# Kernel tuning notes

Measured on AMD Instinct MI355X. Metric: run time of the kernel, lower is better.

The kernel has to match this reference:

```python
import jax, jax.numpy as jnp
import numpy as np

K = 2
NOISE_STD = 1.0

def setup_inputs() -> dict:
    key = jax.random.key(0)
    k1, k2, k3 = jax.random.split(key, 3)
    N, D, E = 131072, 1024, 64
    x = jax.random.normal(k1, (N, D), dtype=jnp.float32)
    W = jax.random.normal(k2, (E, D), dtype=jnp.float32) * (1.0 / np.sqrt(D))
    b = jnp.zeros((E,), dtype=jnp.float32)
    noise = jax.random.normal(k3, (N, E), dtype=jnp.float32)
    return {"x": x, "W": W, "b": b, "noise": noise}

def reference(x, W, b, noise) -> jnp.ndarray:
    # clean logits: [N, E]
    clean_logits = jnp.einsum('nd,ed->ne', x, W) + b
    noisy_logits = clean_logits + noise * NOISE_STD
    topk_vals, topk_idx = jax.lax.top_k(noisy_logits, K)  # [N, K]
    topk_softmax = jax.nn.softmax(topk_vals, axis=-1)     # [N, K]
    rows = jnp.arange(x.shape[0])[:, None]                 # [N, 1]
    gate_weights = jnp.zeros_like(clean_logits).at[rows, topk_idx].set(topk_softmax)
    return gate_weights
```

## Files before the change

kernel.cpp:

```cpp
#include <hip/hip_runtime.h>
#include <math.h>


#define NEXP   64
#define BLOCK  256
#define TILE_M 64
#define DFIX   1024
#define KCF    128
#define NCH    8
#define XCHB   32768
#define TAU    1e-3f
#define CAP    4096
#define WS_W_OFF 32768

typedef __attribute__((ext_vector_type(8)))  short bf16x8;
typedef __attribute__((ext_vector_type(16))) float f32x16;

__device__ __forceinline__ bool beats(float v, int e, float vo, int eo) {
    return (v > vo) || (v == vo && e < eo);
}

__device__ __forceinline__ void split2(float f0, float f1, unsigned int& hi, unsigned int& lo) {
    unsigned int u0 = __float_as_uint(f0), u1 = __float_as_uint(f1);
    unsigned int h0 = u0 & 0xFFFF0000u,  h1 = u1 & 0xFFFF0000u;
    float l0 = f0 - __uint_as_float(h0);
    float l1 = f1 - __uint_as_float(h1);
    hi = (u0 >> 16) | h1;
    lo = (__float_as_uint(l0) >> 16) | (__float_as_uint(l1) & 0xFFFF0000u);
}

__device__ __forceinline__ void gl_lds16(const void* g, void* l) {
    __builtin_amdgcn_global_load_lds((const __attribute__((address_space(1))) void*)g,
                                     (__attribute__((address_space(3))) void*)l,
                                     16, 0, 0);
}

__global__ void convW_kernel(const float* __restrict__ W, char* __restrict__ wsW) {
    const int e = blockIdx.x;
    const int t = threadIdx.x;
    const float* wp = W + e * DFIX + t * 8;
    float4 a  = *(const float4*)wp;
    float4 bq = *(const float4*)(wp + 4);
    unsigned int h[4], l[4];
    split2(a.x,  a.y,  h[0], l[0]);
    split2(a.z,  a.w,  h[1], l[1]);
    split2(bq.x, bq.y, h[2], l[2]);
    split2(bq.z, bq.w, h[3], l[3]);
    const int kk   = t >> 1;
    const int lh   = t & 1;
    const int lane = lh * 32 + (e & 31);
    const int g    = e >> 5;
    char* base = wsW + (size_t)(kk * 4 + g * 2) * 1024 + lane * 16;
    *(uint4*)(base)        = make_uint4(h[0], h[1], h[2], h[3]);
    *(uint4*)(base + 1024) = make_uint4(l[0], l[1], l[2], l[3]);
}

__global__ __launch_bounds__(BLOCK, 2)
void gate_mfma(const float* __restrict__ x, const float* __restrict__ bvec,
               const float* __restrict__ noise, const char* __restrict__ wsW,
               float* __restrict__ out, unsigned int* __restrict__ flags) {
    __shared__ __align__(16) char lds[2 * XCHB];

    const int tid  = threadIdx.x;
    const int wv   = tid >> 6;
    const int lane = tid & 63;
    const int e0   = lane & 31;
    const int lh   = lane >> 5;
    const int rg   = wv & 1;
    const int cg   = wv >> 1;
    const int blkRow0 = blockIdx.x * TILE_M;
    const int rowL  = rg * 32 + e0;
    const int phase = blockIdx.x & (NCH - 1);

    f32x16 acc = (f32x16)0.0f;

    auto STAGE = [&](int gc, int buf) {
        char* xb = lds + buf * XCHB;
        #pragma unroll
        for (int j = 0; j < 8; j++) {
            const int s   = j * 256 + wv * 64 + lane;
            const int row = s >> 5;
            const int seg = (s & 31) ^ (row & 31);
            const char* gp = (const char*)(x + (size_t)(blkRow0 + row) * DFIX)
                             + (size_t)gc * 512 + seg * 16;
            gl_lds16(gp, xb + (size_t)(j * 256 + wv * 64) * 16);
        }
    };

    int4 wreg[16];
    auto WPRE = [&](int gc) {
        const char* base = wsW + (size_t)(gc * 32 + cg * 2) * 1024 + lane * 16;
        #pragma unroll
        for (int ks = 0; ks < 8; ks++) {
            wreg[ks * 2 + 0] = *(const int4*)(base + (ks * 4 + 0) * 1024);
            wreg[ks * 2 + 1] = *(const int4*)(base + (ks * 4 + 1) * 1024);
        }
    };

    auto COMPUTE = [&](int buf) {
        const char* xb = lds + buf * XCHB;
        #pragma unroll
        for (int ks = 0; ks < 8; ks++) {
            const int g0 = ks * 4 + lh * 2;
            const int4 xq0 = *(const int4*)(xb + rowL * 512 + ((g0    ) ^ (rowL & 31)) * 16);
            const int4 xq1 = *(const int4*)(xb + rowL * 512 + ((g0 + 1) ^ (rowL & 31)) * 16);
            const float4 xa = *(const float4*)&xq0;
            const float4 xc = *(const float4*)&xq1;
            union { bf16x8 v; unsigned int u[4]; } ah, al;
            split2(xa.x, xa.y, ah.u[0], al.u[0]);
            split2(xa.z, xa.w, ah.u[1], al.u[1]);
            split2(xc.x, xc.y, ah.u[2], al.u[2]);
            split2(xc.z, xc.w, ah.u[3], al.u[3]);
            union { bf16x8 v; int4 q; } bh, bl;
            bh.q = wreg[ks * 2 + 0];
            bl.q = wreg[ks * 2 + 1];
            acc = __builtin_amdgcn_mfma_f32_32x32x16_bf16(ah.v, bh.v, acc, 0, 0, 0);
            acc = __builtin_amdgcn_mfma_f32_32x32x16_bf16(ah.v, bl.v, acc, 0, 0, 0);
            acc = __builtin_amdgcn_mfma_f32_32x32x16_bf16(al.v, bh.v, acc, 0, 0, 0);
        }
    };

    STAGE(phase, 0);
    #pragma unroll 1
    for (int c = 0; c < NCH - 1; c++) {
        WPRE((c + phase) & (NCH - 1));
        STAGE((c + 1 + phase) & (NCH - 1), (c + 1) & 1);
        asm volatile("s_waitcnt vmcnt(8)" ::: "memory");
        __builtin_amdgcn_s_barrier();
        __builtin_amdgcn_sched_barrier(0);
        COMPUTE(c & 1);
        __builtin_amdgcn_s_barrier();
    }
    WPRE((NCH - 1 + phase) & (NCH - 1));
    asm volatile("s_waitcnt vmcnt(0)" ::: "memory");
    __builtin_amdgcn_s_barrier();
    __builtin_amdgcn_sched_barrier(0);
    COMPUTE((NCH - 1) & 1);

    const float bb = bvec[cg * 32 + e0];
    #pragma unroll
    for (int q = 0; q < 4; q++) {
        #pragma unroll
        for (int j = 0; j < 4; j++) {
            const int reg = q * 4 + j;
            const int rl  = rg * 32 + j + 8 * q + 4 * lh;
            const int r   = blkRow0 + rl;
            const int col = cg * 32 + e0;
            const float v = (acc[reg] + bb) + noise[(size_t)r * NEXP + col];
            const int slot = (col >> 2) ^ (rl & 15);
            *(float*)(lds + rl * 256 + slot * 16 + (col & 3) * 4) = v;
        }
    }
    __syncthreads();

    {
        const int trow = tid >> 2;
        const int qd   = tid & 3;
        float v1 = -1e30f, v2 = -1e30f, v3 = -1e30f;
        int   e1 = 99, e2 = 99;
        #pragma unroll
        for (int i = 0; i < 4; i++) {
            const int slot = (qd * 4 + i) ^ (trow & 15);
            const float4 f = *(const float4*)(lds + trow * 256 + slot * 16);
            #pragma unroll
            for (int m = 0; m < 4; m++) {
                const float v = (m == 0) ? f.x : (m == 1) ? f.y : (m == 2) ? f.z : f.w;
                const int   e = qd * 16 + i * 4 + m;
                if (beats(v, e, v1, e1))      { v3 = v2; v2 = v1; e2 = e1; v1 = v; e1 = e; }
                else if (beats(v, e, v2, e2)) { v3 = v2; v2 = v;  e2 = e; }
                else                          { v3 = fmaxf(v3, v); }
            }
        }
        #pragma unroll
        for (int d = 1; d < 4; d <<= 1) {
            float ov1 = __shfl_xor(v1, d); int oe1 = __shfl_xor(e1, d);
            float ov2 = __shfl_xor(v2, d); int oe2 = __shfl_xor(e2, d);
            float ov3 = __shfl_xor(v3, d);
            bool  aw  = beats(v1, e1, ov1, oe1);
            float a1v = aw ? v1 : ov1; int a1e = aw ? e1 : oe1;
            float b1v = aw ? ov1 : v1; int b1e = aw ? oe1 : e1;
            float a2v = aw ? v2 : ov2; int a2e = aw ? e2 : oe2;
            float b2v = aw ? ov2 : v2;
            float a3v = aw ? v3 : ov3;
            bool  s2  = beats(a2v, a2e, b1v, b1e);
            v1 = a1v; e1 = a1e;
            v2 = s2 ? a2v : b1v; e2 = s2 ? a2e : b1e;
            v3 = s2 ? fmaxf(a3v, b1v) : fmaxf(a2v, b2v);
        }
        const float t   = __expf(v2 - v1);
        const float inv = 1.0f / (1.0f + t);
        const float w1  = inv, w2 = t * inv;
        const int   r   = blkRow0 + trow;

        if (qd == 0 && (v2 - v3) < TAU) {
            unsigned int idx = atomicAdd(flags, 1u);
            if (idx < CAP) flags[1 + idx] = (unsigned int)r;
        }
        float* op = out + (size_t)r * NEXP + qd * 16;
        #pragma unroll
        for (int i = 0; i < 4; i++) {
            float o[4];
            #pragma unroll
            for (int m = 0; m < 4; m++) {
                const int e = qd * 16 + i * 4 + m;
                o[m] = (e == e1) ? w1 : (e == e2) ? w2 : 0.0f;
            }
            *(float4*)(op + i * 4) = make_float4(o[0], o[1], o[2], o[3]);
        }
    }
}

__global__ void gate_repair(const float* __restrict__ x, const float* __restrict__ W,
                            const float* __restrict__ b, const float* __restrict__ noise,
                            float* __restrict__ out, const unsigned int* __restrict__ flags,
                            int D) {
    unsigned int cnt = flags[0];
    if (cnt > CAP) cnt = CAP;
    if (blockIdx.x >= cnt) return;
    const int r = (int)flags[1 + blockIdx.x];
    const int e = threadIdx.x;

    const float* xr = x + (size_t)r * D;
    const float* wr = W + (size_t)e * D;
    double s = 0.0;
    for (int d0 = 0; d0 < D; d0 += 4) {
        float4 xv = *(const float4*)(xr + d0);
        float4 wv = *(const float4*)(wr + d0);
        s += (double)xv.x * (double)wv.x;
        s += (double)xv.y * (double)wv.y;
        s += (double)xv.z * (double)wv.z;
        s += (double)xv.w * (double)wv.w;
    }
    const float clean = (float)s + b[e];
    const float v     = clean + noise[(size_t)r * NEXP + e];

    float v1 = v, v2 = -1e30f; int e1 = e, e2 = 99;
    for (int d = 1; d < 64; d <<= 1) {
        float ov1 = __shfl_xor(v1, d); int oe1 = __shfl_xor(e1, d);
        float ov2 = __shfl_xor(v2, d); int oe2 = __shfl_xor(e2, d);
        bool  aw  = beats(v1, e1, ov1, oe1);
        float a1v = aw ? v1 : ov1; int a1e = aw ? e1 : oe1;
        float b1v = aw ? ov1 : v1; int b1e = aw ? oe1 : e1;
        float a2v = aw ? v2 : ov2; int a2e = aw ? e2 : oe2;
        bool  s2  = beats(a2v, a2e, b1v, b1e);
        v1 = a1v; e1 = a1e;
        v2 = s2 ? a2v : b1v; e2 = s2 ? a2e : b1e;
    }
    const float t   = __expf(v2 - v1);
    const float inv = 1.0f / (1.0f + t);
    out[(size_t)r * NEXP + e] = (e == e1) ? inv : (e == e2) ? t * inv : 0.0f;
}

extern "C" void kernel_launch(void* const* d_in, const int* in_sizes, int n_in,
                              void* d_out, int out_size, void* d_ws, size_t ws_size,
                              hipStream_t stream) {
    const float* x     = (const float*)d_in[0];
    const float* W     = (const float*)d_in[1];
    const float* b     = (const float*)d_in[2];
    const float* noise = (const float*)d_in[3];
    float* out = (float*)d_out;

    const int E = in_sizes[2];
    const int D = in_sizes[1] / E;
    const int N = in_sizes[0] / D;

    unsigned int* flags = (unsigned int*)d_ws;
    char* wsW = (char*)d_ws + WS_W_OFF;

    convW_kernel<<<dim3(E), dim3(128), 0, stream>>>(W, wsW);
    hipMemsetAsync(d_ws, 0, sizeof(unsigned int), stream);
    gate_mfma<<<dim3(N / TILE_M), dim3(BLOCK), 0, stream>>>(x, b, noise, wsW, out, flags);
    gate_repair<<<dim3(CAP), dim3(64), 0, stream>>>(x, W, b, noise, out, flags, D);
}
```

Baseline: 204.8 us.

## Double K-chunk size to 256 and load W fragments inline during compute

Each staged x chunk now covers 256 columns instead of 128, giving four pipeline stages instead of eight and a 128 KB double-buffered LDS footprint, with occupancy lowered to one block per CU. The register-prefetched W fragments are dropped and W is read from global memory inside the compute loop right before each MFMA. The intent is fewer barriers and larger, better-amortized loads, but it gives up occupancy and puts W global-load latency directly on the MFMA path.

```diff
diff --git a/kernel.cpp b/kernel.cpp
--- a/kernel.cpp
+++ b/kernel.cpp
@@ -6,9 +6,9 @@
 #define BLOCK  256
 #define TILE_M 64
 #define DFIX   1024
-#define KCF    128
-#define NCH    8
-#define XCHB   32768
+#define KCF    256
+#define NCH    4
+#define XCHB   65536
 #define TAU    1e-3f
 #define CAP    4096
 #define WS_W_OFF 32768
@@ -55,7 +55,7 @@
     *(uint4*)(base + 1024) = make_uint4(l[0], l[1], l[2], l[3]);
 }
 
-__global__ __launch_bounds__(BLOCK, 2)
+__global__ __launch_bounds__(BLOCK, 1)
 void gate_mfma(const float* __restrict__ x, const float* __restrict__ bvec,
                const float* __restrict__ noise, const char* __restrict__ wsW,
                float* __restrict__ out, unsigned int* __restrict__ flags) {
@@ -77,33 +77,27 @@
     auto STAGE = [&](int gc, int buf) {
         char* xb = lds + buf * XCHB;
         #pragma unroll
-        for (int j = 0; j < 8; j++) {
-            const int s   = j * 256 + wv * 64 + lane;
-            const int row = s >> 5;
-            const int seg = (s & 31) ^ (row & 31);
+        for (int i = 0; i < 16; i++) {
+            const int row = wv * 16 + i;
+            const int seg = lane ^ row;
             const char* gp = (const char*)(x + (size_t)(blkRow0 + row) * DFIX)
-                             + (size_t)gc * 512 + seg * 16;
-            gl_lds16(gp, xb + (size_t)(j * 256 + wv * 64) * 16);
+                             + (size_t)gc * 1024 + seg * 16;
+            gl_lds16(gp, xb + (size_t)(wv * 1024 + i * 64) * 16);
         }
     };
 
-    int4 wreg[16];
-    auto WPRE = [&](int gc) {
-        const char* base = wsW + (size_t)(gc * 32 + cg * 2) * 1024 + lane * 16;
-        #pragma unroll
-        for (int ks = 0; ks < 8; ks++) {
-            wreg[ks * 2 + 0] = *(const int4*)(base + (ks * 4 + 0) * 1024);
-            wreg[ks * 2 + 1] = *(const int4*)(base + (ks * 4 + 1) * 1024);
-        }
-    };
-
-    auto COMPUTE = [&](int buf) {
+    auto COMPUTE = [&](int gc, int buf) {
         const char* xb = lds + buf * XCHB;
         #pragma unroll
-        for (int ks = 0; ks < 8; ks++) {
+        for (int ks = 0; ks < 16; ks++) {
+            const int kkg = gc * 16 + ks;
+            const char* wbase = wsW + (size_t)(kkg * 4 + cg * 2) * 1024 + lane * 16;
+            union { bf16x8 v; int4 q; } bh, bl;
+            bh.q = *(const int4*)(wbase);
+            bl.q = *(const int4*)(wbase + 1024);
             const int g0 = ks * 4 + lh * 2;
-            const int4 xq0 = *(const int4*)(xb + rowL * 512 + ((g0    ) ^ (rowL & 31)) * 16);
-            const int4 xq1 = *(const int4*)(xb + rowL * 512 + ((g0 + 1) ^ (rowL & 31)) * 16);
+            const int4 xq0 = *(const int4*)(xb + rowL * 1024 + ((g0    ) ^ rowL) * 16);
+            const int4 xq1 = *(const int4*)(xb + rowL * 1024 + ((g0 + 1) ^ rowL) * 16);
             const float4 xa = *(const float4*)&xq0;
             const float4 xc = *(const float4*)&xq1;
             union { bf16x8 v; unsigned int u[4]; } ah, al;
@@ -111,9 +105,6 @@
             split2(xa.z, xa.w, ah.u[1], al.u[1]);
             split2(xc.x, xc.y, ah.u[2], al.u[2]);
             split2(xc.z, xc.w, ah.u[3], al.u[3]);
-            union { bf16x8 v; int4 q; } bh, bl;
-            bh.q = wreg[ks * 2 + 0];
-            bl.q = wreg[ks * 2 + 1];
             acc = __builtin_amdgcn_mfma_f32_32x32x16_bf16(ah.v, bh.v, acc, 0, 0, 0);
             acc = __builtin_amdgcn_mfma_f32_32x32x16_bf16(ah.v, bl.v, acc, 0, 0, 0);
             acc = __builtin_amdgcn_mfma_f32_32x32x16_bf16(al.v, bh.v, acc, 0, 0, 0);
@@ -123,19 +114,17 @@
     STAGE(phase, 0);
     #pragma unroll 1
     for (int c = 0; c < NCH - 1; c++) {
-        WPRE((c + phase) & (NCH - 1));
         STAGE((c + 1 + phase) & (NCH - 1), (c + 1) & 1);
-        asm volatile("s_waitcnt vmcnt(8)" ::: "memory");
+        asm volatile("s_waitcnt vmcnt(16)" ::: "memory");
         __builtin_amdgcn_s_barrier();
         __builtin_amdgcn_sched_barrier(0);
-        COMPUTE(c & 1);
+        COMPUTE((c + phase) & (NCH - 1), c & 1);
         __builtin_amdgcn_s_barrier();
     }
-    WPRE((NCH - 1 + phase) & (NCH - 1));
     asm volatile("s_waitcnt vmcnt(0)" ::: "memory");
     __builtin_amdgcn_s_barrier();
     __builtin_amdgcn_sched_barrier(0);
-    COMPUTE((NCH - 1) & 1);
+    COMPUTE((NCH - 1 + phase) & (NCH - 1), (NCH - 1) & 1);
 
     const float bb = bvec[cg * 32 + e0];
     #pragma unroll
```

Result: slower. 314.8 us (+53.7%).

## Halve row tile and split K across waves with LDS reduction

Applied to the files above, without the earlier changes.

Shrinks the row tile from 64 to 32 rows. The four waves now split the K dimension in two halves and the expert columns in two halves, and the two K-halves are summed through LDS before the bias, noise and top-k epilogue. This doubles the grid size and widens each staged chunk to 256 columns across 4 chunks. The aim is more blocks for occupancy and load balance, at the cost of an extra LDS reduction and more barriers, with each W fragment reused over fewer rows. Scheduling barriers are also added around the prefetch and staging code.

```diff
diff --git a/kernel.cpp b/kernel.cpp
--- a/kernel.cpp
+++ b/kernel.cpp
@@ -4,11 +4,11 @@
 
 #define NEXP   64
 #define BLOCK  256
-#define TILE_M 64
+#define TILE_M 32
 #define DFIX   1024
-#define KCF    128
-#define NCH    8
+#define NCH    4
 #define XCHB   32768
+#define TK_OFF 8192
 #define TAU    1e-3f
 #define CAP    4096
 #define WS_W_OFF 32768
@@ -66,10 +66,10 @@
     const int lane = tid & 63;
     const int e0   = lane & 31;
     const int lh   = lane >> 5;
-    const int rg   = wv & 1;
-    const int cg   = wv >> 1;
+    const int cg   = wv & 1;
+    const int kh   = wv >> 1;
     const int blkRow0 = blockIdx.x * TILE_M;
-    const int rowL  = rg * 32 + e0;
+    const int rowL  = e0;
     const int phase = blockIdx.x & (NCH - 1);
 
     f32x16 acc = (f32x16)0.0f;
@@ -77,23 +77,23 @@
     auto STAGE = [&](int gc, int buf) {
         char* xb = lds + buf * XCHB;
         #pragma unroll
-        for (int j = 0; j < 8; j++) {
-            const int s   = j * 256 + wv * 64 + lane;
-            const int row = s >> 5;
-            const int seg = (s & 31) ^ (row & 31);
+        for (int i = 0; i < 8; i++) {
+            const int row = wv * 8 + i;
+            const int seg = lane ^ row;
             const char* gp = (const char*)(x + (size_t)(blkRow0 + row) * DFIX)
-                             + (size_t)gc * 512 + seg * 16;
-            gl_lds16(gp, xb + (size_t)(j * 256 + wv * 64) * 16);
+                             + (size_t)gc * 1024 + seg * 16;
+            gl_lds16(gp, xb + (size_t)(row * 64) * 16);
         }
     };
 
     int4 wreg[16];
     auto WPRE = [&](int gc) {
-        const char* base = wsW + (size_t)(gc * 32 + cg * 2) * 1024 + lane * 16;
+        const int kk0 = gc * 16 + kh * 8;
+        const char* base = wsW + (size_t)(kk0 * 4 + cg * 2) * 1024 + lane * 16;
         #pragma unroll
         for (int ks = 0; ks < 8; ks++) {
-            wreg[ks * 2 + 0] = *(const int4*)(base + (ks * 4 + 0) * 1024);
-            wreg[ks * 2 + 1] = *(const int4*)(base + (ks * 4 + 1) * 1024);
+            wreg[ks * 2 + 0] = *(const int4*)(base + (size_t)(ks * 4) * 1024);
+            wreg[ks * 2 + 1] = *(const int4*)(base + (size_t)(ks * 4) * 1024 + 1024);
         }
     };
 
@@ -101,9 +101,10 @@
         const char* xb = lds + buf * XCHB;
         #pragma unroll
         for (int ks = 0; ks < 8; ks++) {
-            const int g0 = ks * 4 + lh * 2;
-            const int4 xq0 = *(const int4*)(xb + rowL * 512 + ((g0    ) ^ (rowL & 31)) * 16);
-            const int4 xq1 = *(const int4*)(xb + rowL * 512 + ((g0 + 1) ^ (rowL & 31)) * 16);
+            const int ksc = kh * 8 + ks;
+            const int g0  = ksc * 4 + lh * 2;
+            const int4 xq0 = *(const int4*)(xb + rowL * 1024 + ((g0    ) ^ rowL) * 16);
+            const int4 xq1 = *(const int4*)(xb + rowL * 1024 + ((g0 + 1) ^ rowL) * 16);
             const float4 xa = *(const float4*)&xq0;
             const float4 xc = *(const float4*)&xq1;
             union { bf16x8 v; unsigned int u[4]; } ah, al;
@@ -124,7 +125,9 @@
     #pragma unroll 1
     for (int c = 0; c < NCH - 1; c++) {
         WPRE((c + phase) & (NCH - 1));
+        __builtin_amdgcn_sched_barrier(0);
         STAGE((c + 1 + phase) & (NCH - 1), (c + 1) & 1);
+        __builtin_amdgcn_sched_barrier(0);
         asm volatile("s_waitcnt vmcnt(8)" ::: "memory");
         __builtin_amdgcn_s_barrier();
         __builtin_amdgcn_sched_barrier(0);
@@ -137,42 +140,61 @@
     __builtin_amdgcn_sched_barrier(0);
     COMPUTE((NCH - 1) & 1);
 
-    const float bb = bvec[cg * 32 + e0];
-    #pragma unroll
-    for (int q = 0; q < 4; q++) {
-        #pragma unroll
-        for (int j = 0; j < 4; j++) {
-            const int reg = q * 4 + j;
-            const int rl  = rg * 32 + j + 8 * q + 4 * lh;
-            const int r   = blkRow0 + rl;
-            const int col = cg * 32 + e0;
-            const float v = (acc[reg] + bb) + noise[(size_t)r * NEXP + col];
-            const int slot = (col >> 2) ^ (rl & 15);
-            *(float*)(lds + rl * 256 + slot * 16 + (col & 3) * 4) = v;
-        }
-    }
     __syncthreads();
+    union { f32x16 v; float4 f4[4]; } au; au.v = acc;
+    if (kh == 1) {
+        #pragma unroll
+        for (int r4 = 0; r4 < 4; r4++)
+            *(float4*)(lds + cg * 4096 + r4 * 1024 + lane * 16) = au.f4[r4];
+    }
+    __syncthreads();
+    if (kh == 0) {
+        #pragma unroll
+        for (int r4 = 0; r4 < 4; r4++) {
+            const float4 t = *(const float4*)(lds + cg * 4096 + r4 * 1024 + lane * 16);
+            au.f4[r4].x += t.x; au.f4[r4].y += t.y; au.f4[r4].z += t.z; au.f4[r4].w += t.w;
+        }
+        const float bb = bvec[cg * 32 + e0];
+        #pragma unroll
+        for (int q = 0; q < 4; q++) {
+            #pragma unroll
+            for (int j = 0; j < 4; j++) {
+                const int reg = q * 4 + j;
+                const int rl  = j + 8 * q + 4 * lh;
+                const int r   = blkRow0 + rl;
+                const int col = cg * 32 + e0;
+                const float v = (au.f4[reg >> 2].x * 0.0f) +
+                                ((reg & 3) == 0 ? au.f4[reg >> 2].x :
+                                 (reg & 3) == 1 ? au.f4[reg >> 2].y :
+                                 (reg & 3) == 2 ? au.f4[reg >> 2].z : au.f4[reg >> 2].w)
+                                + bb + noise[(size_t)r * NEXP + col];
+                const int slot = (col >> 2) ^ (rl & 15);
+                *(float*)(lds + TK_OFF + rl * 256 + slot * 16 + (col & 3) * 4) = v;
+            }
+        }
+    }
+    __syncthreads();
 
     {
-        const int trow = tid >> 2;
-        const int qd   = tid & 3;
+        const int trow = tid >> 3;
+        const int oct  = tid & 7;
         float v1 = -1e30f, v2 = -1e30f, v3 = -1e30f;
         int   e1 = 99, e2 = 99;
         #pragma unroll
-        for (int i = 0; i < 4; i++) {
-            const int slot = (qd * 4 + i) ^ (trow & 15);
-            const float4 f = *(const float4*)(lds + trow * 256 + slot * 16);
+        for (int i = 0; i < 2; i++) {
+            const int slot = (oct * 2 + i) ^ (trow & 15);
+            const float4 f = *(const float4*)(lds + TK_OFF + trow * 256 + slot * 16);
             #pragma unroll
             for (int m = 0; m < 4; m++) {
                 const float v = (m == 0) ? f.x : (m == 1) ? f.y : (m == 2) ? f.z : f.w;
-                const int   e = qd * 16 + i * 4 + m;
+                const int   e = oct * 8 + i * 4 + m;
                 if (beats(v, e, v1, e1))      { v3 = v2; v2 = v1; e2 = e1; v1 = v; e1 = e; }
                 else if (beats(v, e, v2, e2)) { v3 = v2; v2 = v;  e2 = e; }
                 else                          { v3 = fmaxf(v3, v); }
             }
         }
         #pragma unroll
-        for (int d = 1; d < 4; d <<= 1) {
+        for (int d = 1; d < 8; d <<= 1) {
             float ov1 = __shfl_xor(v1, d); int oe1 = __shfl_xor(e1, d);
             float ov2 = __shfl_xor(v2, d); int oe2 = __shfl_xor(e2, d);
             float ov3 = __shfl_xor(v3, d);
@@ -192,17 +214,17 @@
         const float w1  = inv, w2 = t * inv;
         const int   r   = blkRow0 + trow;
 
-        if (qd == 0 && (v2 - v3) < TAU) {
+        if (oct == 0 && (v2 - v3) < TAU) {
             unsigned int idx = atomicAdd(flags, 1u);
             if (idx < CAP) flags[1 + idx] = (unsigned int)r;
         }
-        float* op = out + (size_t)r * NEXP + qd * 16;
-        #pragma unroll
-        for (int i = 0; i < 4; i++) {
+        float* op = out + (size_t)r * NEXP + oct * 8;
+        #pragma unroll
+        for (int i = 0; i < 2; i++) {
             float o[4];
             #pragma unroll
             for (int m = 0; m < 4; m++) {
-                const int e = qd * 16 + i * 4 + m;
+                const int e = oct * 8 + i * 4 + m;
                 o[m] = (e == e1) ? w1 : (e == e2) ? w2 : 0.0f;
             }
             *(float4*)(op + i * 4) = make_float4(o[0], o[1], o[2], o[3]);
```

Result: slower. 229.4 us (+12.0%).
